# Performance work log

Measured on AMD Instinct MI355X. Metric: run time of the kernel, lower is better.

## Reference

```python
import jax, jax.numpy as jnp
import numpy as np

DIM = 1024
NUM_HEADS = 16
HEAD_DIM = DIM // NUM_HEADS  # 64; only used for the softmax scale


def setup_inputs() -> dict:
    key = jax.random.key(0)
    ks = jax.random.split(key, 9)
    s = 1.0 / np.sqrt(DIM)
    return {
        "x": jax.random.normal(ks[0], (2, 4096, DIM), dtype=jnp.float32),
        "Wq": jax.random.normal(ks[1], (DIM, DIM), dtype=jnp.float32) * s,
        "bq": jnp.zeros((DIM,), dtype=jnp.float32),
        "Wk": jax.random.normal(ks[2], (DIM, DIM), dtype=jnp.float32) * s,
        "bk": jnp.zeros((DIM,), dtype=jnp.float32),
        "Wv": jax.random.normal(ks[3], (DIM, DIM), dtype=jnp.float32) * s,
        "bv": jnp.zeros((DIM,), dtype=jnp.float32),
        "Wo": jax.random.normal(ks[4], (DIM, DIM), dtype=jnp.float32) * s,
        "bo": jnp.zeros((DIM,), dtype=jnp.float32),
    }


def reference(x, Wq, bq, Wk, bk, Wv, bv, Wo, bo):
    # Projections (nn.Linear equivalents)
    q = jnp.einsum("bsd,df->bsf", x, Wq) + bq
    k = jnp.einsum("bsd,df->bsf", x, Wk) + bk
    v = jnp.einsum("bsd,df->bsf", x, Wv) + bv
    # Full-dim attention (no head split); scale uses head_dim per original code.
    scale = 1.0 / np.sqrt(HEAD_DIM)
    scores = jnp.einsum("bqd,bkd->bqk", q, k) * scale  # [B, S, S]
    attn = jax.nn.softmax(scores, axis=-1)
    out = jnp.einsum("bqk,bkd->bqd", attn, v)
    return jnp.einsum("bsd,df->bsf", out, Wo) + bo
```

## Files before the change

### kernel.cpp

```cpp
#include <hip/hip_runtime.h>

typedef unsigned short u16;
using bf16x8  = __attribute__((ext_vector_type(8))) __bf16;
using floatx4 = __attribute__((ext_vector_type(4))) float;

__device__ __forceinline__ u16 f2bf(float f) {
  unsigned int u = __builtin_bit_cast(unsigned int, f);
  u += 0x7fffu + ((u >> 16) & 1u);
  return (u16)(u >> 16);
}
__device__ __forceinline__ float bf2f(u16 h) {
  unsigned int u = ((unsigned int)h) << 16;
  return __builtin_bit_cast(float, u);
}

#define AS1(p) ((const __attribute__((address_space(1))) void*)(p))
#define AS3(p) ((__attribute__((address_space(3))) void*)(p))

#define GEMM_PROLOGUE_AT(bmv, bnv)                                           \
  __shared__ u16 As[128 * 32];                                               \
  __shared__ u16 Bs[128 * 32];                                               \
  const int tid  = threadIdx.x;                                              \
  const int wave = tid >> 6, lane = tid & 63;                                \
  const int wm = (wave >> 1) * 64, wn = (wave & 1) * 64;                     \
  const long bm = (bmv), bn = (bnv);                                         \
  floatx4 acc[4][4] = {};                                                    \
  const int srow = lane >> 2;                                                \
  const int scol = (lane & 3) * 8;                                           \
  const int c0 = wave * 2, c1 = c0 + 1;                                      \
  const int fr = lane & 15;                                                  \
  const int kq = (lane >> 4) * 8;                                            \
  const int oc = (lane >> 4) * 4;

#define GEMM_PROLOGUE() GEMM_PROLOGUE_AT((long)blockIdx.y * 128, (long)blockIdx.x * 128)

#define GEMM_STAGE(Ab, Bb, K, k0)                                            \
    __syncthreads();                                                         \
    __builtin_amdgcn_global_load_lds(AS1(Ab + (long)(c0*16 + srow)*K + k0 + scol), AS3(As + c0*512), 16, 0, 0); \
    __builtin_amdgcn_global_load_lds(AS1(Ab + (long)(c1*16 + srow)*K + k0 + scol), AS3(As + c1*512), 16, 0, 0); \
    __builtin_amdgcn_global_load_lds(AS1(Bb + (long)(c0*16 + srow)*K + k0 + scol), AS3(Bs + c0*512), 16, 0, 0); \
    __builtin_amdgcn_global_load_lds(AS1(Bb + (long)(c1*16 + srow)*K + k0 + scol), AS3(Bs + c1*512), 16, 0, 0); \
    __syncthreads();                                                         \
    bf16x8 af[4], bfv[4];                                                    \
    _Pragma("unroll")                                                        \
    for (int mi = 0; mi < 4; ++mi)                                           \
      af[mi] = *(const bf16x8*)(As + (wm + mi*16 + fr)*32 + kq);             \
    _Pragma("unroll")                                                        \
    for (int ni = 0; ni < 4; ++ni)                                           \
      bfv[ni] = *(const bf16x8*)(Bs + (wn + ni*16 + fr)*32 + kq);

#define GEMM_KSTEP(Ab, Bb, K, k0)                                            \
  {                                                                          \
    GEMM_STAGE(Ab, Bb, K, k0)                                                \
    _Pragma("unroll")                                                        \
    for (int mi = 0; mi < 4; ++mi)                                           \
      _Pragma("unroll")                                                      \
      for (int ni = 0; ni < 4; ++ni)                                         \
        acc[mi][ni] = __builtin_amdgcn_mfma_f32_16x16x32_bf16(af[mi], bfv[ni], acc[mi][ni], 0, 0, 0); \
  }

#define GEMM_KSTEP_SWAP(Ab, Bb, K, k0)                                       \
  {                                                                          \
    GEMM_STAGE(Ab, Bb, K, k0)                                                \
    _Pragma("unroll")                                                        \
    for (int mi = 0; mi < 4; ++mi)                                           \
      _Pragma("unroll")                                                      \
      for (int ni = 0; ni < 4; ++ni)                                         \
        acc[mi][ni] = __builtin_amdgcn_mfma_f32_16x16x32_bf16(bfv[ni], af[mi], acc[mi][ni], 0, 0, 0); \
  }

__global__ __launch_bounds__(256) void gemm_bt(
    const u16* __restrict__ A, const u16* __restrict__ Bt,
    float* __restrict__ Cout, const float* __restrict__ bias, int N, int K)
{
  GEMM_PROLOGUE();
  const u16* Ab = A + bm * K;
  const u16* Bb = Bt + bn * K;
  for (int k0 = 0; k0 < K; k0 += 32) GEMM_KSTEP_SWAP(Ab, Bb, K, k0);

#pragma unroll
  for (int mi = 0; mi < 4; ++mi) {
    long row = bm + wm + mi*16 + fr;
#pragma unroll
    for (int ni = 0; ni < 4; ++ni) {
      long colb = bn + wn + ni*16 + oc;
      float4 bv4 = *(const float4*)(bias + colb);
      float4 o;
      o.x = acc[mi][ni][0] + bv4.x;
      o.y = acc[mi][ni][1] + bv4.y;
      o.z = acc[mi][ni][2] + bv4.z;
      o.w = acc[mi][ni][3] + bv4.w;
      *(float4*)(Cout + row * N + colb) = o;
    }
  }
}

__global__ __launch_bounds__(256) void gemm_qk_exp(
    const u16* __restrict__ q, const u16* __restrict__ k,
    u16* __restrict__ probs, float* __restrict__ lpartT, float alpha)
{
  const int N = 4096, K = 1024;
  const int lin = blockIdx.x + (blockIdx.y << 5) + (blockIdx.z << 10);
  const int xcd = lin & 7, j = lin >> 3;
  const long b = xcd >> 2;
  const int band = (xcd & 3) * 8;
  const int t = j >> 6, w = j & 63;
  const int bx = t * 8 + (w & 7);
  const int by = band + (w >> 3);

  const u16* A  = q + b * 4096 * 1024;
  const u16* Bt = k + b * 4096 * 1024;
  u16* P = probs + b * 4096L * 4096;
  float* lp = lpartT + b * 4096 * 64;

  GEMM_PROLOGUE_AT((long)by * 128, (long)bx * 128);
  const u16* Ab = A + bm * K;
  const u16* Bb = Bt + bn * K;
  for (int k0 = 0; k0 < K; k0 += 32) GEMM_KSTEP_SWAP(Ab, Bb, K, k0);

  float rowsum[4] = {0.f, 0.f, 0.f, 0.f};
#pragma unroll
  for (int mi = 0; mi < 4; ++mi) {
    long row = bm + wm + mi*16 + fr;
#pragma unroll
    for (int ni = 0; ni < 4; ++ni) {
      long colb = bn + wn + ni*16 + oc;
      float e0 = __expf(acc[mi][ni][0] * alpha);
      float e1 = __expf(acc[mi][ni][1] * alpha);
      float e2 = __expf(acc[mi][ni][2] * alpha);
      float e3 = __expf(acc[mi][ni][3] * alpha);
      rowsum[mi] += (e0 + e1) + (e2 + e3);
      ushort4 o;
      o.x = f2bf(e0); o.y = f2bf(e1); o.z = f2bf(e2); o.w = f2bf(e3);
      *(ushort4*)(P + row * N + colb) = o;
    }
  }
  const long cg = bx * 2 + (wn >> 6);
#pragma unroll
  for (int mi = 0; mi < 4; ++mi) {
    float s = rowsum[mi];
    s += __shfl_xor(s, 16); s += __shfl_xor(s, 32);
    if (lane < 16)
      lp[(bm + wm + mi*16 + lane) * 64 + cg] = s;
  }
}

__global__ __launch_bounds__(256) void gemm_qkv(
    const u16* __restrict__ A, const u16* __restrict__ Bt,
    u16* __restrict__ qb, u16* __restrict__ kb, u16* __restrict__ vT,
    const float* __restrict__ bq, const float* __restrict__ bk,
    const float* __restrict__ bv)
{
  const int K = 1024;
  GEMM_PROLOGUE();
  const u16* Ab = A + bm * K;
  const u16* Bb = Bt + bn * K;

  if (bn < 2048) {
    for (int k0 = 0; k0 < K; k0 += 32) GEMM_KSTEP_SWAP(Ab, Bb, K, k0);
    u16* C = (bn < 1024) ? qb : kb;
    const float* bias = (bn < 1024) ? bq : bk;
#pragma unroll
    for (int mi = 0; mi < 4; ++mi) {
      long row = bm + wm + mi*16 + fr;
#pragma unroll
      for (int ni = 0; ni < 4; ++ni) {
        long colg = bn + wn + ni*16 + oc;
        long cc = colg & 1023;
        float4 bv4 = *(const float4*)(bias + cc);
        ushort4 o;
        o.x = f2bf(acc[mi][ni][0] + bv4.x);
        o.y = f2bf(acc[mi][ni][1] + bv4.y);
        o.z = f2bf(acc[mi][ni][2] + bv4.z);
        o.w = f2bf(acc[mi][ni][3] + bv4.w);
        *(ushort4*)(C + row * 1024 + cc) = o;
      }
    }
  } else {
    for (int k0 = 0; k0 < K; k0 += 32) GEMM_KSTEP(Ab, Bb, K, k0);
    const int orow = (lane >> 4) * 4;
    const int ocol = lane & 15;
#pragma unroll
    for (int ni = 0; ni < 4; ++ni) {
      long col = bn + wn + ni*16 + ocol;
      float bvv = bv[col - 2048];
#pragma unroll
      for (int mi = 0; mi < 4; ++mi) {
        long row = bm + wm + mi*16 + orow;
        long b_ = row >> 12, s = row & 4095, d = col - 2048;
        ushort4 o;
        o.x = f2bf(acc[mi][ni][0] + bvv);
        o.y = f2bf(acc[mi][ni][1] + bvv);
        o.z = f2bf(acc[mi][ni][2] + bvv);
        o.w = f2bf(acc[mi][ni][3] + bvv);
        *(ushort4*)(vT + b_ * (1024L * 4096) + d * 4096L + s) = o;
      }
    }
  }
}

__global__ __launch_bounds__(256) void gemm_pv_splitk(
    const u16* __restrict__ probs, const u16* __restrict__ vT,
    u16* __restrict__ pA, u16* __restrict__ pB)
{
  const int N = 1024, K = 4096, Ks = 1024;
  const int lin = blockIdx.x + (blockIdx.y << 3) + (blockIdx.z << 8);
  const int xcd = lin & 7, j = lin >> 3;
  const long b = xcd >> 2;
  const int sp = xcd & 3;
  const int bx = j & 7;
  const int by = j >> 3;

  const u16* A  = probs + b * 4096L * 4096;
  const u16* Bt = vT + b * 1024L * 4096;
  u16* part = (b ? pB : pA) + (long)sp * 4096 * 1024;

  GEMM_PROLOGUE_AT((long)by * 128, (long)bx * 128);
  const u16* Ab = A + bm * K;
  const u16* Bb = Bt + bn * K;
  const int kbeg = sp * Ks, kend = kbeg + Ks;
  for (int k0 = kbeg; k0 < kend; k0 += 32) GEMM_KSTEP_SWAP(Ab, Bb, K, k0);

#pragma unroll
  for (int mi = 0; mi < 4; ++mi) {
    long row = bm + wm + mi*16 + fr;
#pragma unroll
    for (int ni = 0; ni < 4; ++ni) {
      long colb = bn + wn + ni*16 + oc;
      ushort4 o;
      o.x = f2bf(acc[mi][ni][0]);
      o.y = f2bf(acc[mi][ni][1]);
      o.z = f2bf(acc[mi][ni][2]);
      o.w = f2bf(acc[mi][ni][3]);
      *(ushort4*)(part + row * N + colb) = o;
    }
  }
}

__global__ __launch_bounds__(256) void reduce4_div_row(
    const u16* __restrict__ pA, const u16* __restrict__ pB,
    const float* __restrict__ lpartT, u16* __restrict__ ob)
{
  const int row = blockIdx.x;
  const long b = blockIdx.y;
  const int tid = threadIdx.x;
  const u16* part = b ? pB : pA;
  const float* lp = lpartT + b * 4096 * 64;
  __shared__ float sl;
  if (tid < 64) {
    float s = lp[(long)row * 64 + tid];
#pragma unroll
    for (int off = 32; off; off >>= 1) s += __shfl_down(s, off);
    if (tid == 0) sl = s;
  }
  __syncthreads();
  const float inv = 1.0f / sl;
  const long base = (long)row * 1024 + tid * 4;
  float acc4[4] = {0.f, 0.f, 0.f, 0.f};
#pragma unroll
  for (int s = 0; s < 4; ++s) {
    ushort4 p = *(const ushort4*)(part + (long)s * 4096 * 1024 + base);
    acc4[0] += bf2f(p.x); acc4[1] += bf2f(p.y);
    acc4[2] += bf2f(p.z); acc4[3] += bf2f(p.w);
  }
  ushort4 o;
  o.x = f2bf(acc4[0] * inv);
  o.y = f2bf(acc4[1] * inv);
  o.z = f2bf(acc4[2] * inv);
  o.w = f2bf(acc4[3] * inv);
  *(ushort4*)(ob + b * 4096L * 1024 + base) = o;
}

__global__ __launch_bounds__(256) void prep(
    const float* __restrict__ x, u16* __restrict__ xb,
    const float* __restrict__ W0, const float* __restrict__ W1,
    const float* __restrict__ W2, const float* __restrict__ W3,
    u16* __restrict__ O0, u16* __restrict__ O1,
    u16* __restrict__ O2, u16* __restrict__ O3)
{
  __shared__ float tile[32][33];
  int blk = blockIdx.x;
  if (blk < 8192) {
    int i = blk * 256 + threadIdx.x;
    float4 f = ((const float4*)x)[i];
    ushort4 o;
    o.x = f2bf(f.x); o.y = f2bf(f.y); o.z = f2bf(f.z); o.w = f2bf(f.w);
    ((ushort4*)xb)[i] = o;
  } else {
    blk -= 8192;
    const int z = blk >> 10, t = blk & 1023;
    const float* in = (z == 0) ? W0 : (z == 1) ? W1 : (z == 2) ? W2 : W3;
    u16* outp = (z == 0) ? O0 : (z == 1) ? O1 : (z == 2) ? O2 : O3;
    const int bx = (t & 31) * 32, by = (t >> 5) * 32;
    const int tx = threadIdx.x & 31, ty = threadIdx.x >> 5;
    for (int i = ty; i < 32; i += 8)
      tile[i][tx] = in[(long)(by + i) * 1024 + bx + tx];
    __syncthreads();
    for (int i = ty; i < 32; i += 8)
      outp[(long)(bx + i) * 1024 + by + tx] = f2bf(tile[tx][i]);
  }
}

extern "C" void kernel_launch(void* const* d_in, const int* in_sizes, int n_in,
                              void* d_out, int out_size, void* d_ws, size_t ws_size,
                              hipStream_t stream) {
  const float* x  = (const float*)d_in[0];
  const float* Wq = (const float*)d_in[1];
  const float* bq = (const float*)d_in[2];
  const float* Wk = (const float*)d_in[3];
  const float* bk = (const float*)d_in[4];
  const float* Wv = (const float*)d_in[5];
  const float* bv = (const float*)d_in[6];
  const float* Wo = (const float*)d_in[7];
  const float* bo = (const float*)d_in[8];
  float* out = (float*)d_out;

  const int B = 2, S = 4096, D = 1024;
  const long MS = (long)B * S;
  const long MB = 1L << 20;

  char* w = (char*)d_ws;
  u16* qb  = (u16*)(w);
  u16* kb  = (u16*)(w + 16 * MB);
  u16* vT  = (u16*)(w + 32 * MB);
  u16* xb  = (u16*)(w + 48 * MB);
  u16* ob  = xb;
  u16* WqkvT = (u16*)(w + 64 * MB);
  u16* WoT = WqkvT + 3072L * 1024;
  u16* probs = (u16*)(w + 72 * MB);
  u16* partA = (u16*)(w);
  u16* partB = (u16*)(w + 136 * MB);
  float* lpartT = (float*)d_out;

  prep<<<dim3(8192 + 4096), 256, 0, stream>>>(
      x, xb, Wq, Wk, Wv, Wo,
      WqkvT, WqkvT + 1024L * 1024, WqkvT + 2048L * 1024, WoT);

  gemm_qkv<<<dim3(3 * D / 128, MS / 128), 256, 0, stream>>>(
      xb, WqkvT, qb, kb, vT, bq, bk, bv);

  const float scale = 0.125f;
  gemm_qk_exp<<<dim3(S / 128, S / 128, B), 256, 0, stream>>>(
      qb, kb, probs, lpartT, scale);
  gemm_pv_splitk<<<dim3(D / 128, S / 128, 8), 256, 0, stream>>>(
      probs, vT, partA, partB);
  reduce4_div_row<<<dim3(S, B), 256, 0, stream>>>(partA, partB, lpartT, ob);

  gemm_bt<<<dim3(D / 128, MS / 128), 256, 0, stream>>>(ob, WoT, out, bo, D, D);
}
```

Baseline: 410.2 us.

## Use 256x256 multi-buffered async-LDS GEMM for QK-exp and PV split-K

Replaces the 128x128 GEMM tiles of the QK^T-exp and PV kernels with 512-thread 256x256 tiles. These use a four-slot LDS ring filled by global_load_lds, with explicit vmcnt waits, barriers and setprio to overlap loads with MFMA. PV split-K drops from 4 to 2 slices, so the reduce kernel sums only two partials. Exp switches to the native exp2 with a pre-scaled alpha. This should raise arithmetic intensity and hide memory latency, but uses 128 KB of LDS, fewer blocks and hand-tuned wait counts that are fragile.

Result: faster. 385.2 us (-6.1%).

```diff
diff --git a/kernel.cpp b/kernel.cpp
--- a/kernel.cpp
+++ b/kernel.cpp
@@ -69,6 +69,93 @@
         acc[mi][ni] = __builtin_amdgcn_mfma_f32_16x16x32_bf16(bfv[ni], af[mi], acc[mi][ni], 0, 0, 0); \
   }
 
+#define NE_PROLOGUE(bmv, bnv)                                                \
+  __shared__ u16 lds[65536];                                    \
+  const int tid = threadIdx.x;                                               \
+  const int w = tid >> 6, lane = tid & 63;                                   \
+  const int wm = (w >> 2) * 128, wn = (w & 3) * 64;                          \
+  const int wm16 = (w >> 2) * 8;           \
+  const int wn4  = (w & 3) * 4;            \
+  const long bm = (bmv), bn = (bnv);                                         \
+  floatx4 acc[8][4] = {};                                                    \
+  const int fr = lane & 15;                                                  \
+  const int kq = (lane >> 4) * 8;                                            \
+  const int oc = (lane >> 4) * 4;                                            \
+         \
+  const int swz  = (lane * 16) ^ (((lane >> 5) & 1) << 5);                   \
+  const int srow = swz >> 6;                  \
+  const int scol = (swz & 63) >> 1;           \
+  const int st0  = w * 2;                      \
+                        \
+  const int aoff = fr * 64 + ((kq * 2) ^ (((fr >> 3) & 1) << 5));
+
+#define NE_SETUP_PTRS(Abp, Bbp, ldK)                                         \
+  const u16* A0p = (Abp) + (long)(st0 * 16 + srow) * (ldK) + scol;           \
+  const u16* A1p = A0p + 16L * (ldK);                                        \
+  const u16* B0p = (Bbp) + (long)(st0 * 16 + srow) * (ldK) + scol;           \
+  const u16* B1p = B0p + 16L * (ldK);
+
+#define NE_SA(T)                                                             \
+  { u16* d_ = lds + (((T) & 3) * 16384) + st0 * 512;                         \
+    long o_ = (long)(T) * 32;                                                \
+    __builtin_amdgcn_global_load_lds(AS1(A0p + o_), AS3(d_), 16, 0, 0);      \
+    __builtin_amdgcn_global_load_lds(AS1(A1p + o_), AS3(d_ + 512), 16, 0, 0); }
+#define NE_SB(T)                                                             \
+  { u16* d_ = lds + (((T) & 3) * 16384) + 8192 + st0 * 512;                  \
+    long o_ = (long)(T) * 32;                                                \
+    __builtin_amdgcn_global_load_lds(AS1(B0p + o_), AS3(d_), 16, 0, 0);      \
+    __builtin_amdgcn_global_load_lds(AS1(B1p + o_), AS3(d_ + 512), 16, 0, 0); }
+
+#define NE_TILE(T, NT)                                                       \
+  {                                                                          \
+    const char* sb_ = (const char*)lds + ((T) & 3) * 32768;                  \
+    bf16x8 af[4], bf[4];                                                     \
+    _Pragma("unroll")                                                        \
+    for (int i = 0; i < 4; ++i)                                              \
+      af[i] = *(const bf16x8*)(sb_ + (wm16 + i) * 1024 + aoff);              \
+    _Pragma("unroll")                                                        \
+    for (int i = 0; i < 4; ++i)                                              \
+      bf[i] = *(const bf16x8*)(sb_ + 16384 + (wn4 + i) * 1024 + aoff);       \
+    if ((T) + 2 < (NT)) NE_SB((T) + 2)                                       \
+    __builtin_amdgcn_s_barrier();                                            \
+    asm volatile("s_waitcnt lgkmcnt(0)" ::: "memory");                       \
+    __builtin_amdgcn_sched_barrier(0);                                       \
+    __builtin_amdgcn_s_setprio(1);                                           \
+    _Pragma("unroll")                                                        \
+    for (int mi = 0; mi < 4; ++mi)                                           \
+      _Pragma("unroll")                                                      \
+      for (int ni = 0; ni < 4; ++ni)                                         \
+        acc[mi][ni] = __builtin_amdgcn_mfma_f32_16x16x32_bf16(bf[ni], af[mi], acc[mi][ni], 0, 0, 0); \
+    __builtin_amdgcn_s_setprio(0);                                           \
+    __builtin_amdgcn_s_barrier();                                            \
+    __builtin_amdgcn_sched_barrier(0);                                       \
+    _Pragma("unroll")                                                        \
+    for (int i = 0; i < 4; ++i)                                              \
+      af[i] = *(const bf16x8*)(sb_ + (wm16 + 4 + i) * 1024 + aoff);          \
+    if ((T) + 3 < (NT)) NE_SA((T) + 3)                                       \
+    __builtin_amdgcn_s_barrier();                                            \
+    asm volatile("s_waitcnt lgkmcnt(0)" ::: "memory");                       \
+    __builtin_amdgcn_sched_barrier(0);                                       \
+    __builtin_amdgcn_s_setprio(1);                                           \
+    _Pragma("unroll")                                                        \
+    for (int mi = 0; mi < 4; ++mi)                                           \
+      _Pragma("unroll")                                                      \
+      for (int ni = 0; ni < 4; ++ni)                                         \
+        acc[4 + mi][ni] = __builtin_amdgcn_mfma_f32_16x16x32_bf16(bf[ni], af[mi], acc[4 + mi][ni], 0, 0, 0); \
+    __builtin_amdgcn_s_setprio(0);                                           \
+    if ((T) < (NT) - 3)       { asm volatile("s_waitcnt vmcnt(6)" ::: "memory"); } \
+    else if ((T) == (NT) - 3) { asm volatile("s_waitcnt vmcnt(4)" ::: "memory"); } \
+    else if ((T) == (NT) - 2) { asm volatile("s_waitcnt vmcnt(0)" ::: "memory"); } \
+    __builtin_amdgcn_s_barrier();                                            \
+    __builtin_amdgcn_sched_barrier(0);                                       \
+  }
+
+#define NE_START()                                                           \
+  NE_SA(0) NE_SB(0) NE_SA(1) NE_SB(1) NE_SA(2)                               \
+  asm volatile("s_waitcnt vmcnt(6)" ::: "memory");                           \
+  __builtin_amdgcn_s_barrier();                                              \
+  __builtin_amdgcn_sched_barrier(0);
+
 __global__ __launch_bounds__(256) void gemm_bt(
     const u16* __restrict__ A, const u16* __restrict__ Bt,
     float* __restrict__ Cout, const float* __restrict__ bias, int N, int K)
@@ -95,53 +182,85 @@
   }
 }
 
-__global__ __launch_bounds__(256) void gemm_qk_exp(
+__global__ __launch_bounds__(512, 2) void gemm_qk_exp(
     const u16* __restrict__ q, const u16* __restrict__ k,
     u16* __restrict__ probs, float* __restrict__ lpartT, float alpha)
 {
-  const int N = 4096, K = 1024;
-  const int lin = blockIdx.x + (blockIdx.y << 5) + (blockIdx.z << 10);
-  const int xcd = lin & 7, j = lin >> 3;
+  const int N = 4096;
+  const int xcd = blockIdx.x;
+  const int j = blockIdx.y;
   const long b = xcd >> 2;
-  const int band = (xcd & 3) * 8;
-  const int t = j >> 6, w = j & 63;
-  const int bx = t * 8 + (w & 7);
-  const int by = band + (w >> 3);
-
-  const u16* A  = q + b * 4096 * 1024;
-  const u16* Bt = k + b * 4096 * 1024;
+  const int by = (xcd & 3) * 4 + (j & 3);
+  const int bx = j >> 2;
+
+  NE_PROLOGUE((long)by * 256, (long)bx * 256);
+  const u16* Ab = q + b * 4096 * 1024 + bm * 1024;
+  const u16* Bb = k + b * 4096 * 1024 + bn * 1024;
+  NE_SETUP_PTRS(Ab, Bb, 1024);
   u16* P = probs + b * 4096L * 4096;
   float* lp = lpartT + b * 4096 * 64;
 
-  GEMM_PROLOGUE_AT((long)by * 128, (long)bx * 128);
-  const u16* Ab = A + bm * K;
-  const u16* Bb = Bt + bn * K;
-  for (int k0 = 0; k0 < K; k0 += 32) GEMM_KSTEP_SWAP(Ab, Bb, K, k0);
-
-  float rowsum[4] = {0.f, 0.f, 0.f, 0.f};
-#pragma unroll
-  for (int mi = 0; mi < 4; ++mi) {
-    long row = bm + wm + mi*16 + fr;
+  NE_START()
+  for (int T = 0; T < 32; ++T) NE_TILE(T, 32)
+
+  const float a2 = alpha * 1.44269504f;
+  const int cg = bx * 4 + (w & 3);
+#pragma unroll
+  for (int mi = 0; mi < 8; ++mi) {
+    long row = bm + wm + mi * 16 + fr;
+    float rs = 0.f;
 #pragma unroll
     for (int ni = 0; ni < 4; ++ni) {
-      long colb = bn + wn + ni*16 + oc;
-      float e0 = __expf(acc[mi][ni][0] * alpha);
-      float e1 = __expf(acc[mi][ni][1] * alpha);
-      float e2 = __expf(acc[mi][ni][2] * alpha);
-      float e3 = __expf(acc[mi][ni][3] * alpha);
-      rowsum[mi] += (e0 + e1) + (e2 + e3);
+      long colb = bn + wn + ni * 16 + oc;
+      float e0 = __builtin_amdgcn_exp2f(acc[mi][ni][0] * a2);
+      float e1 = __builtin_amdgcn_exp2f(acc[mi][ni][1] * a2);
+      float e2 = __builtin_amdgcn_exp2f(acc[mi][ni][2] * a2);
+      float e3 = __builtin_amdgcn_exp2f(acc[mi][ni][3] * a2);
+      rs += (e0 + e1) + (e2 + e3);
       ushort4 o;
       o.x = f2bf(e0); o.y = f2bf(e1); o.z = f2bf(e2); o.w = f2bf(e3);
       *(ushort4*)(P + row * N + colb) = o;
     }
-  }
-  const long cg = bx * 2 + (wn >> 6);
-#pragma unroll
-  for (int mi = 0; mi < 4; ++mi) {
-    float s = rowsum[mi];
-    s += __shfl_xor(s, 16); s += __shfl_xor(s, 32);
+    rs += __shfl_xor(rs, 16);
+    rs += __shfl_xor(rs, 32);
     if (lane < 16)
-      lp[(bm + wm + mi*16 + lane) * 64 + cg] = s;
+      lp[(bm + wm + mi * 16 + lane) * 64 + cg] = rs;
+  }
+}
+
+__global__ __launch_bounds__(512, 2) void gemm_pv_splitk2(
+    const u16* __restrict__ probs, const u16* __restrict__ vT,
+    u16* __restrict__ pA, u16* __restrict__ pB)
+{
+  const int xcd = blockIdx.x;
+  const int j = blockIdx.y;
+  const long b = xcd >> 2;
+  const int sp = (xcd >> 1) & 1;
+  const int by = (xcd & 1) * 8 + (j & 7);
+  const int bx = j >> 3;
+
+  NE_PROLOGUE((long)by * 256, (long)bx * 256);
+  const u16* Ab = probs + b * 4096L * 4096 + bm * 4096 + sp * 2048;
+  const u16* Bb = vT + b * 1024L * 4096 + bn * 4096 + sp * 2048;
+  NE_SETUP_PTRS(Ab, Bb, 4096);
+  u16* part = (b ? pB : pA) + (long)sp * 4096 * 1024;
+
+  NE_START()
+  for (int T = 0; T < 64; ++T) NE_TILE(T, 64)
+
+#pragma unroll
+  for (int mi = 0; mi < 8; ++mi) {
+    long row = bm + wm + mi * 16 + fr;
+#pragma unroll
+    for (int ni = 0; ni < 4; ++ni) {
+      long colb = bn + wn + ni * 16 + oc;
+      ushort4 o;
+      o.x = f2bf(acc[mi][ni][0]);
+      o.y = f2bf(acc[mi][ni][1]);
+      o.z = f2bf(acc[mi][ni][2]);
+      o.w = f2bf(acc[mi][ni][3]);
+      *(ushort4*)(part + row * 1024 + colb) = o;
+    }
   }
 }
 
@@ -199,45 +318,7 @@
   }
 }
 
-__global__ __launch_bounds__(256) void gemm_pv_splitk(
-    const u16* __restrict__ probs, const u16* __restrict__ vT,
-    u16* __restrict__ pA, u16* __restrict__ pB)
-{
-  const int N = 1024, K = 4096, Ks = 1024;
-  const int lin = blockIdx.x + (blockIdx.y << 3) + (blockIdx.z << 8);
-  const int xcd = lin & 7, j = lin >> 3;
-  const long b = xcd >> 2;
-  const int sp = xcd & 3;
-  const int bx = j & 7;
-  const int by = j >> 3;
-
-  const u16* A  = probs + b * 4096L * 4096;
-  const u16* Bt = vT + b * 1024L * 4096;
-  u16* part = (b ? pB : pA) + (long)sp * 4096 * 1024;
-
-  GEMM_PROLOGUE_AT((long)by * 128, (long)bx * 128);
-  const u16* Ab = A + bm * K;
-  const u16* Bb = Bt + bn * K;
-  const int kbeg = sp * Ks, kend = kbeg + Ks;
-  for (int k0 = kbeg; k0 < kend; k0 += 32) GEMM_KSTEP_SWAP(Ab, Bb, K, k0);
-
-#pragma unroll
-  for (int mi = 0; mi < 4; ++mi) {
-    long row = bm + wm + mi*16 + fr;
-#pragma unroll
-    for (int ni = 0; ni < 4; ++ni) {
-      long colb = bn + wn + ni*16 + oc;
-      ushort4 o;
-      o.x = f2bf(acc[mi][ni][0]);
-      o.y = f2bf(acc[mi][ni][1]);
-      o.z = f2bf(acc[mi][ni][2]);
-      o.w = f2bf(acc[mi][ni][3]);
-      *(ushort4*)(part + row * N + colb) = o;
-    }
-  }
-}
-
-__global__ __launch_bounds__(256) void reduce4_div_row(
+__global__ __launch_bounds__(256) void reduce2_div_row(
     const u16* __restrict__ pA, const u16* __restrict__ pB,
     const float* __restrict__ lpartT, u16* __restrict__ ob)
 {
@@ -258,7 +339,7 @@
   const long base = (long)row * 1024 + tid * 4;
   float acc4[4] = {0.f, 0.f, 0.f, 0.f};
 #pragma unroll
-  for (int s = 0; s < 4; ++s) {
+  for (int s = 0; s < 2; ++s) {
     ushort4 p = *(const ushort4*)(part + (long)s * 4096 * 1024 + base);
     acc4[0] += bf2f(p.x); acc4[1] += bf2f(p.y);
     acc4[2] += bf2f(p.z); acc4[3] += bf2f(p.w);
@@ -340,11 +421,11 @@
       xb, WqkvT, qb, kb, vT, bq, bk, bv);
 
   const float scale = 0.125f;
-  gemm_qk_exp<<<dim3(S / 128, S / 128, B), 256, 0, stream>>>(
+  gemm_qk_exp<<<dim3(8, 64), 512, 0, stream>>>(
       qb, kb, probs, lpartT, scale);
-  gemm_pv_splitk<<<dim3(D / 128, S / 128, 8), 256, 0, stream>>>(
+  gemm_pv_splitk2<<<dim3(8, 32), 512, 0, stream>>>(
       probs, vT, partA, partB);
-  reduce4_div_row<<<dim3(S, B), 256, 0, stream>>>(partA, partB, lpartT, ob);
+  reduce2_div_row<<<dim3(S, B), 256, 0, stream>>>(partA, partB, lpartT, ob);
 
   gemm_bt<<<dim3(D / 128, MS / 128), 256, 0, stream>>>(ob, WoT, out, bo, D, D);
 }
```
